# Performance work log

Measured on AMD Instinct MI355X. Metric: run time of the kernel, lower is better.

The kernel has to match this reference:

```python
import jax, jax.numpy as jnp
import numpy as np

NUM_HEADS = 12
EPS = 1e-4


def setup_inputs() -> dict:
    key = jax.random.key(0)
    k1, k2, k3 = jax.random.split(key, 3)
    C = 768
    B, N = 128, 196  # B = b * num_frames = 8 * 16
    x = jax.random.normal(k1, (B, N, C), dtype=jnp.float32)
    W_qkv = jax.random.normal(k2, (3 * C, C), dtype=jnp.float32) * 0.02
    W_proj = jax.random.normal(k3, (C, C), dtype=jnp.float32) * 0.02
    b_proj = jnp.zeros((C,), dtype=jnp.float32)
    return {"x": x, "W_qkv": W_qkv, "W_proj": W_proj, "b_proj": b_proj,
            "num_frames": 16}


def reference(x, W_qkv, W_proj, b_proj, num_frames):
    B, N, C = x.shape
    h = NUM_HEADS
    e = C // h
    # qkv projection (no bias), split k-first then heads: 'b n (k h e)'
    qkv = (x @ W_qkv.T).reshape(B, N, 3, h, e)
    q, k, v = qkv[:, :, 0], qkv[:, :, 1], qkv[:, :, 2]  # [B, N, h, e]
    q_ = jax.nn.relu(q)
    k_ = jax.nn.relu(k)
    # fold frames into the sequence: (b f) n -> b (f n)
    b = B // num_frames
    S = num_frames * N
    q_ = q_.reshape(b, S, h, e)
    k_ = k_.reshape(b, S, h, e)
    v_ = v.reshape(b, S, h, e)
    # kv trick: kv[b,h,e,d] = sum_s k[b,s,h,e] v[b,s,h,d]
    kv = jnp.einsum('bshe,bshd->bhed', k_, v_)
    k_sum = k_.sum(axis=1)  # [b, h, e]
    z = 1.0 / (jnp.einsum('bshe,bhe->bsh', q_, k_sum) + EPS)  # [b, S, h]
    out = jnp.einsum('bshe,bhed->bshd', q_, kv) * z[..., None]  # [b, S, h, e]
    out = out.reshape(B, N, C)
    # output projection (dropouts are identity at eval)
    return out @ W_proj.T + b_proj
```

## Files before the change

kernel.cpp:

```cpp
#include <hip/hip_runtime.h>
#include <hip/hip_bf16.h>

#define EPS_Z 1e-4f

typedef __attribute__((ext_vector_type(8))) short bf16x8;
typedef __attribute__((ext_vector_type(4))) float f32x4;

__device__ __forceinline__ float b2f(short s) {
    union { unsigned u; float f; } cv;
    cv.u = ((unsigned)(unsigned short)s) << 16;
    return cv.f;
}

__device__ __forceinline__ void gld_lds16(const __hip_bfloat16* g, __hip_bfloat16* l) {
    __builtin_amdgcn_global_load_lds(
        (__attribute__((address_space(1))) void*)(g),
        (__attribute__((address_space(3))) void*)(l),
        16, 0, 0);
}

__global__ __launch_bounds__(256)
void cvt_all(const float* __restrict__ x, const float* __restrict__ wq,
             const float* __restrict__ wp,
             __hip_bfloat16* __restrict__ xb, __hip_bfloat16* __restrict__ wqb,
             __hip_bfloat16* __restrict__ wpb)
{
    const int N4X = 25088 * 768 / 4;
    const int N4Q = 2304 * 768 / 4;
    const int N4P = 768 * 768 / 4;
    int i = blockIdx.x * 256 + threadIdx.x;
    const float* src;
    __hip_bfloat16* dst;
    int idx;
    if (i < N4X)            { src = x;  dst = xb;  idx = i; }
    else if (i < N4X + N4Q) { src = wq; dst = wqb; idx = i - N4X; }
    else if (i < N4X + N4Q + N4P) { src = wp; dst = wpb; idx = i - N4X - N4Q; }
    else return;
    float4 v = ((const float4*)src)[idx];
    union { short4 s; __hip_bfloat16 h[4]; } o;
    o.h[0] = __float2bfloat16(v.x);
    o.h[1] = __float2bfloat16(v.y);
    o.h[2] = __float2bfloat16(v.z);
    o.h[3] = __float2bfloat16(v.w);
    ((short4*)dst)[idx] = o.s;
}

template<int MODE, typename CT>
__global__ __launch_bounds__(256, 4)
void gemm_bt(const __hip_bfloat16* __restrict__ A,
             const __hip_bfloat16* __restrict__ B,
             CT* __restrict__ C,
             const float* __restrict__ bias,
             int K, int N, int gx)
{
    __shared__ __align__(16) __hip_bfloat16 As[128 * 64];
    __shared__ __align__(16) __hip_bfloat16 Bs[128 * 64];
    const int nwg = (int)gridDim.x;
    const int g = blockIdx.x;
    const int xcd = g & 7, lin = g >> 3;
    const int q = nwg >> 3, r = nwg & 7;
    const int gp = (xcd < r ? xcd * (q + 1) : r * (q + 1) + (xcd - r) * q) + lin;
    const int bx = gp % gx;
    const int by = gp / gx;

    const int tid = threadIdx.x;
    const int w = tid >> 6;
    const int l = tid & 63;
    const int wr = (w >> 1) * 64;
    const int wc = (w & 1) * 64;
    const int l15 = l & 15;
    const int lq = l >> 4;
    const int rx = l15 & 7;

    f32x4 acc[4][4] = {};

    const int srow8 = l >> 3;
    const int scol = (((l & 7) ^ (l >> 3)) << 3);

    const __hip_bfloat16* Ab = A + (size_t)by * 128 * K;
    const __hip_bfloat16* Bb = B + (size_t)bx * 128 * K;

    for (int k0 = 0; k0 < K; k0 += 64) {
        __syncthreads();
        #pragma unroll
        for (int i = 0; i < 4; ++i) {
            const int chunk = w * 4 + i;
            const int row = chunk * 8 + srow8;
            gld_lds16(Ab + (size_t)row * K + (k0 + scol), As + chunk * 512);
            gld_lds16(Bb + (size_t)row * K + (k0 + scol), Bs + chunk * 512);
        }
        __syncthreads();
        #pragma unroll
        for (int kk = 0; kk < 64; kk += 32) {
            const int kb = (kk >> 3) + lq;
            const int col = (kb ^ rx) << 3;
            bf16x8 a[4], b[4];
            #pragma unroll
            for (int i = 0; i < 4; ++i)
                a[i] = *(const bf16x8*)(As + (wr + i * 16 + l15) * 64 + col);
            #pragma unroll
            for (int j = 0; j < 4; ++j)
                b[j] = *(const bf16x8*)(Bs + (wc + j * 16 + l15) * 64 + col);
            #pragma unroll
            for (int i = 0; i < 4; ++i)
                #pragma unroll
                for (int j = 0; j < 4; ++j)
                    acc[i][j] = __builtin_amdgcn_mfma_f32_16x16x32_bf16(a[i], b[j], acc[i][j], 0, 0, 0);
        }
    }

    const int crow0 = by * 128 + wr + lq * 4;
    const int ccol0 = bx * 128 + wc + l15;
    #pragma unroll
    for (int i = 0; i < 4; ++i) {
        #pragma unroll
        for (int j = 0; j < 4; ++j) {
            const int gc = ccol0 + j * 16;
            const float badd = (MODE == 2) ? bias[gc] : 0.0f;
            #pragma unroll
            for (int r2 = 0; r2 < 4; ++r2) {
                const int gr = crow0 + i * 16 + r2;
                float v = acc[i][j][r2];
                if (MODE == 1 && gc < 1536) v = fmaxf(v, 0.0f);
                if (MODE == 2) v += badd;
                if (MODE == 1)
                    ((__hip_bfloat16*)C)[(size_t)gr * N + gc] = __float2bfloat16(v);
                else
                    ((float*)C)[(size_t)gr * N + gc] = v;
            }
        }
    }
}

__global__ __launch_bounds__(256)
void kv_mfma_kernel(const __hip_bfloat16* __restrict__ qkv,
                    float* __restrict__ kvp, float* __restrict__ ksump)
{
    const int SPLIT = 7;
    const int bh = blockIdx.x / SPLIT;
    const int ck = blockIdx.x % SPLIT;
    const int b = bh / 12, h = bh % 12;

    __shared__ __align__(16) __hip_bfloat16 kT[64 * 40];
    __shared__ __align__(16) __hip_bfloat16 vT[64 * 40];

    const int tid = threadIdx.x;
    const int w = tid >> 6, l = tid & 63;
    const int l15 = l & 15, lq = l >> 4;

    const int half = tid >> 7;
    const int idx  = tid & 127;
    const int e0 = (idx >> 4) * 8;
    const int sp = idx & 15;

    const size_t rowbase = (size_t)b * 3136 * 2304 + (half ? 1536 : 768) + h * 64 + e0;
    __hip_bfloat16* Tdst = half ? vT : kT;

    f32x4 acc[4] = {};
    f32x4 accks = {};

    bf16x8 ones;
    #pragma unroll
    for (int i = 0; i < 8; ++i) ones[i] = (short)0x3F80;

    const int s_begin = ck * 448;
    const int s_end = s_begin + 448;

    bf16x8 r0 = *(const bf16x8*)(qkv + rowbase + (size_t)(s_begin + 2 * sp) * 2304);
    bf16x8 r1 = *(const bf16x8*)(qkv + rowbase + (size_t)(s_begin + 2 * sp + 1) * 2304);

    for (int s0 = s_begin; s0 < s_end; s0 += 32) {
        __syncthreads();
        #pragma unroll
        for (int qq = 0; qq < 8; ++qq) {
            unsigned pk = ((unsigned)(unsigned short)r0[qq]) |
                          (((unsigned)(unsigned short)r1[qq]) << 16);
            *(unsigned*)(Tdst + (e0 + qq) * 40 + 2 * sp) = pk;
        }
        __syncthreads();
        if (s0 + 32 < s_end) {
            r0 = *(const bf16x8*)(qkv + rowbase + (size_t)(s0 + 32 + 2 * sp) * 2304);
            r1 = *(const bf16x8*)(qkv + rowbase + (size_t)(s0 + 33 + 2 * sp) * 2304);
        }
        bf16x8 a = *(const bf16x8*)(vT + (w * 16 + l15) * 40 + lq * 8);
        bf16x8 bfr[4];
        #pragma unroll
        for (int j = 0; j < 4; ++j)
            bfr[j] = *(const bf16x8*)(kT + (j * 16 + l15) * 40 + lq * 8);
        #pragma unroll
        for (int j = 0; j < 4; ++j)
            acc[j] = __builtin_amdgcn_mfma_f32_16x16x32_bf16(a, bfr[j], acc[j], 0, 0, 0);
        accks = __builtin_amdgcn_mfma_f32_16x16x32_bf16(ones, bfr[w], accks, 0, 0, 0);
    }

    float* kvdst = kvp + ((size_t)(bh * SPLIT + ck) << 12);
    #pragma unroll
    for (int j = 0; j < 4; ++j) {
        const int col = j * 16 + l15;
        #pragma unroll
        for (int r = 0; r < 4; ++r) {
            const int row = w * 16 + lq * 4 + r;
            kvdst[row * 64 + col] = acc[j][r];
        }
    }
    if (lq == 0)
        ksump[(size_t)(bh * SPLIT + ck) * 64 + w * 16 + l15] = accks[0];
}

__global__ __launch_bounds__(256)
void kv_reduce(const float* __restrict__ kvp, const float* __restrict__ ksump,
               __hip_bfloat16* __restrict__ kvb, float* __restrict__ ksum)
{
    const int SPLIT = 7;
    const int bh = blockIdx.x;
    const int tid = threadIdx.x;

    const float* base = kvp + ((size_t)bh * SPLIT << 12) + tid * 16;
    float4 s0 = {}, s1 = {}, s2 = {}, s3 = {};
    #pragma unroll
    for (int p = 0; p < SPLIT; ++p) {
        const float* bp = base + ((size_t)p << 12);
        float4 a0 = *(const float4*)(bp + 0);
        float4 a1 = *(const float4*)(bp + 4);
        float4 a2 = *(const float4*)(bp + 8);
        float4 a3 = *(const float4*)(bp + 12);
        s0.x += a0.x; s0.y += a0.y; s0.z += a0.z; s0.w += a0.w;
        s1.x += a1.x; s1.y += a1.y; s1.z += a1.z; s1.w += a1.w;
        s2.x += a2.x; s2.y += a2.y; s2.z += a2.z; s2.w += a2.w;
        s3.x += a3.x; s3.y += a3.y; s3.z += a3.z; s3.w += a3.w;
    }
    union { bf16x8 v; __hip_bfloat16 h[8]; } o0, o1;
    o0.h[0] = __float2bfloat16(s0.x); o0.h[1] = __float2bfloat16(s0.y);
    o0.h[2] = __float2bfloat16(s0.z); o0.h[3] = __float2bfloat16(s0.w);
    o0.h[4] = __float2bfloat16(s1.x); o0.h[5] = __float2bfloat16(s1.y);
    o0.h[6] = __float2bfloat16(s1.z); o0.h[7] = __float2bfloat16(s1.w);
    o1.h[0] = __float2bfloat16(s2.x); o1.h[1] = __float2bfloat16(s2.y);
    o1.h[2] = __float2bfloat16(s2.z); o1.h[3] = __float2bfloat16(s2.w);
    o1.h[4] = __float2bfloat16(s3.x); o1.h[5] = __float2bfloat16(s3.y);
    o1.h[6] = __float2bfloat16(s3.z); o1.h[7] = __float2bfloat16(s3.w);
    __hip_bfloat16* dst = kvb + ((size_t)bh << 12) + tid * 16;
    *(bf16x8*)(dst + 0) = o0.v;
    *(bf16x8*)(dst + 8) = o1.v;

    if (tid < 64) {
        float t = 0.0f;
        #pragma unroll
        for (int p = 0; p < SPLIT; ++p)
            t += ksump[(size_t)(bh * SPLIT + p) * 64 + tid];
        ksum[(size_t)bh * 64 + tid] = t;
    }
}

__global__ __launch_bounds__(128)
void attn_mfma3(const __hip_bfloat16* __restrict__ qkv,
                const __hip_bfloat16* __restrict__ kvb,
                const float* __restrict__ ksumg,
                __hip_bfloat16* __restrict__ att)
{
    const int x = blockIdx.x;
    const int b = x / 98;
    const int rem = x % 98;
    const int mt = rem >> 1, half = rem & 1;
    const int tid = threadIdx.x;
    const int w = tid >> 6, l = tid & 63;
    const int l15 = l & 15, lq = l >> 4;

    const size_t m0 = (size_t)b * 3136 + (size_t)mt * 64 + half * 32 + w * 16;

    #pragma unroll 1
    for (int h = 0; h < 12; ++h) {
        const int bh = b * 12 + h;

        const __hip_bfloat16* kvh = kvb + ((size_t)bh << 12);
        bf16x8 b0[4], b1[4];
        #pragma unroll
        for (int j = 0; j < 4; ++j) {
            b0[j] = *(const bf16x8*)(kvh + (j * 16 + l15) * 64 + lq * 8);
            b1[j] = *(const bf16x8*)(kvh + (j * 16 + l15) * 64 + 32 + lq * 8);
        }
        const float* ks = ksumg + (bh << 6);
        float kse[8], kse1[8];
        *(float4*)(kse)      = *(const float4*)(ks + lq * 8);
        *(float4*)(kse + 4)  = *(const float4*)(ks + lq * 8 + 4);
        *(float4*)(kse1)     = *(const float4*)(ks + 32 + lq * 8);
        *(float4*)(kse1 + 4) = *(const float4*)(ks + 32 + lq * 8 + 4);

        const __hip_bfloat16* qrow = qkv + (m0 + l15) * 2304 + h * 64;
        bf16x8 aq0 = *(const bf16x8*)(qrow + lq * 8);
        bf16x8 aq1 = *(const bf16x8*)(qrow + 32 + lq * 8);

        float zp = 0.0f;
        #pragma unroll
        for (int j = 0; j < 8; ++j)
            zp += b2f(aq0[j]) * kse[j] + b2f(aq1[j]) * kse1[j];
        zp += __shfl_xor(zp, 16);
        zp += __shfl_xor(zp, 32);
        const float zr = 1.0f / (zp + EPS_Z);

        f32x4 acc[4] = {};
        #pragma unroll
        for (int j = 0; j < 4; ++j) {
            acc[j] = __builtin_amdgcn_mfma_f32_16x16x32_bf16(aq0, b0[j], acc[j], 0, 0, 0);
            acc[j] = __builtin_amdgcn_mfma_f32_16x16x32_bf16(aq1, b1[j], acc[j], 0, 0, 0);
        }

        float zrow[4];
        #pragma unroll
        for (int r = 0; r < 4; ++r) zrow[r] = __shfl(zr, lq * 4 + r);

        #pragma unroll
        for (int j = 0; j < 4; ++j) {
            const int col = j * 16 + l15;
            #pragma unroll
            for (int r = 0; r < 4; ++r) {
                const int row = lq * 4 + r;
                att[(m0 + row) * 768 + h * 64 + col] = __float2bfloat16(acc[j][r] * zrow[r]);
            }
        }
    }
}

extern "C" void kernel_launch(void* const* d_in, const int* in_sizes, int n_in,
                              void* d_out, int out_size, void* d_ws, size_t ws_size,
                              hipStream_t stream)
{
    const float* x      = (const float*)d_in[0];
    const float* W_qkv  = (const float*)d_in[1];
    const float* W_proj = (const float*)d_in[2];
    const float* b_proj = (const float*)d_in[3];
    float* out = (float*)d_out;

    const int M = 25088, K = 768, N1 = 2304, N2 = 768;
    const int SPLIT = 7;
    const int MH = M / 2;

    __hip_bfloat16* qkv = (__hip_bfloat16*)d_ws;
    __hip_bfloat16* xb  = qkv + (size_t)M * N1;
    __hip_bfloat16* wqb = xb + (size_t)M * K;
    __hip_bfloat16* wpb = wqb + (size_t)N1 * K;
    float* kvp   = (float*)(wpb + (size_t)N2 * K);
    float* ksump = kvp + (size_t)SPLIT * 96 * 4096;
    float* ksum  = ksump + (size_t)SPLIT * 96 * 64;
    __hip_bfloat16* kvb = (__hip_bfloat16*)(ksum + 96 * 64);
    __hip_bfloat16* att = xb;

    const int CVT_TOT = (M * K + N1 * K + N2 * K) / 4;
    cvt_all<<<(CVT_TOT + 255) / 256, 256, 0, stream>>>(x, W_qkv, W_proj, xb, wqb, wpb);

    gemm_bt<1, __hip_bfloat16><<<(MH / 128) * (N1 / 128), 256, 0, stream>>>(
        xb, wqb, qkv, nullptr, K, N1, N1 / 128);
    gemm_bt<1, __hip_bfloat16><<<(MH / 128) * (N1 / 128), 256, 0, stream>>>(
        xb + (size_t)MH * K, wqb, qkv + (size_t)MH * N1, nullptr, K, N1, N1 / 128);

    kv_mfma_kernel<<<96 * SPLIT, 256, 0, stream>>>(qkv, kvp, ksump);
    kv_reduce<<<96, 256, 0, stream>>>(kvp, ksump, kvb, ksum);
    attn_mfma3<<<784, 128, 0, stream>>>(qkv, kvb, ksum, att);
    gemm_bt<2, float><<<(M / 128) * (N2 / 128), 256, 0, stream>>>(
        att, wpb, out, b_proj, K, N2, N2 / 128);
}
```

Measured before the change: 360.4 us.

## Fuse attention output with projection GEMM and merge split QKV GEMM launches

```diff
diff --git a/kernel.cpp b/kernel.cpp
--- a/kernel.cpp
+++ b/kernel.cpp
@@ -46,7 +46,7 @@
 }
 
 template<int MODE, typename CT>
-__global__ __launch_bounds__(256, 4)
+__global__ __launch_bounds__(256, 3)
 void gemm_bt(const __hip_bfloat16* __restrict__ A,
              const __hip_bfloat16* __restrict__ B,
              CT* __restrict__ C,
@@ -251,32 +251,35 @@
     }
 }
 
-__global__ __launch_bounds__(128)
-void attn_mfma3(const __hip_bfloat16* __restrict__ qkv,
-                const __hip_bfloat16* __restrict__ kvb,
-                const float* __restrict__ ksumg,
-                __hip_bfloat16* __restrict__ att)
-{
-    const int x = blockIdx.x;
-    const int b = x / 98;
-    const int rem = x % 98;
-    const int mt = rem >> 1, half = rem & 1;
+__global__ __launch_bounds__(256, 3)
+void attn_proj(const __hip_bfloat16* __restrict__ qkv,
+               const __hip_bfloat16* __restrict__ kvb,
+               const float* __restrict__ ksumg,
+               const __hip_bfloat16* __restrict__ wpb,
+               const float* __restrict__ bias,
+               float* __restrict__ out)
+{
+    __shared__ __align__(16) __hip_bfloat16 att_s[32 * 776];
+
+    const int blk = blockIdx.x;
+    const size_t m0 = (size_t)blk * 32;
+    const int bidx = (int)(m0 / 3136);
     const int tid = threadIdx.x;
     const int w = tid >> 6, l = tid & 63;
     const int l15 = l & 15, lq = l >> 4;
-
-    const size_t m0 = (size_t)b * 3136 + (size_t)mt * 64 + half * 32 + w * 16;
+    const int rt = w & 1;
+    const int ch = w >> 1;
 
     #pragma unroll 1
     for (int h = 0; h < 12; ++h) {
-        const int bh = b * 12 + h;
-
+        const int bh = bidx * 12 + h;
         const __hip_bfloat16* kvh = kvb + ((size_t)bh << 12);
-        bf16x8 b0[4], b1[4];
-        #pragma unroll
-        for (int j = 0; j < 4; ++j) {
-            b0[j] = *(const bf16x8*)(kvh + (j * 16 + l15) * 64 + lq * 8);
-            b1[j] = *(const bf16x8*)(kvh + (j * 16 + l15) * 64 + 32 + lq * 8);
+        bf16x8 b0[2], b1[2];
+        #pragma unroll
+        for (int j = 0; j < 2; ++j) {
+            const int col = ch * 32 + j * 16 + l15;
+            b0[j] = *(const bf16x8*)(kvh + col * 64 + lq * 8);
+            b1[j] = *(const bf16x8*)(kvh + col * 64 + 32 + lq * 8);
         }
         const float* ks = ksumg + (bh << 6);
         float kse[8], kse1[8];
@@ -285,7 +288,7 @@
         *(float4*)(kse1)     = *(const float4*)(ks + 32 + lq * 8);
         *(float4*)(kse1 + 4) = *(const float4*)(ks + 32 + lq * 8 + 4);
 
-        const __hip_bfloat16* qrow = qkv + (m0 + l15) * 2304 + h * 64;
+        const __hip_bfloat16* qrow = qkv + (m0 + rt * 16 + l15) * 2304 + h * 64;
         bf16x8 aq0 = *(const bf16x8*)(qrow + lq * 8);
         bf16x8 aq1 = *(const bf16x8*)(qrow + 32 + lq * 8);
 
@@ -297,11 +300,11 @@
         zp += __shfl_xor(zp, 32);
         const float zr = 1.0f / (zp + EPS_Z);
 
-        f32x4 acc[4] = {};
-        #pragma unroll
-        for (int j = 0; j < 4; ++j) {
-            acc[j] = __builtin_amdgcn_mfma_f32_16x16x32_bf16(aq0, b0[j], acc[j], 0, 0, 0);
-            acc[j] = __builtin_amdgcn_mfma_f32_16x16x32_bf16(aq1, b1[j], acc[j], 0, 0, 0);
+        f32x4 pacc[2] = {};
+        #pragma unroll
+        for (int j = 0; j < 2; ++j) {
+            pacc[j] = __builtin_amdgcn_mfma_f32_16x16x32_bf16(aq0, b0[j], pacc[j], 0, 0, 0);
+            pacc[j] = __builtin_amdgcn_mfma_f32_16x16x32_bf16(aq1, b1[j], pacc[j], 0, 0, 0);
         }
 
         float zrow[4];
@@ -309,12 +312,46 @@
         for (int r = 0; r < 4; ++r) zrow[r] = __shfl(zr, lq * 4 + r);
 
         #pragma unroll
-        for (int j = 0; j < 4; ++j) {
-            const int col = j * 16 + l15;
+        for (int j = 0; j < 2; ++j) {
+            const int col = h * 64 + ch * 32 + j * 16 + l15;
             #pragma unroll
             for (int r = 0; r < 4; ++r) {
-                const int row = lq * 4 + r;
-                att[(m0 + row) * 768 + h * 64 + col] = __float2bfloat16(acc[j][r] * zrow[r]);
+                const int row = rt * 16 + lq * 4 + r;
+                att_s[row * 776 + col] = __float2bfloat16(pacc[j][r] * zrow[r]);
+            }
+        }
+    }
+    __syncthreads();
+
+    #pragma unroll 1
+    for (int pass = 0; pass < 2; ++pass) {
+        const int c0 = w * 192 + pass * 96;
+        f32x4 acc[2][6] = {};
+        #pragma unroll 1
+        for (int k0 = 0; k0 < 768; k0 += 32) {
+            bf16x8 a0 = *(const bf16x8*)(att_s + (0 * 16 + l15) * 776 + k0 + lq * 8);
+            bf16x8 a1 = *(const bf16x8*)(att_s + (1 * 16 + l15) * 776 + k0 + lq * 8);
+            bf16x8 bf[6];
+            #pragma unroll
+            for (int j = 0; j < 6; ++j)
+                bf[j] = *(const bf16x8*)(wpb + (size_t)(c0 + j * 16 + l15) * 768 + k0 + lq * 8);
+            #pragma unroll
+            for (int j = 0; j < 6; ++j) {
+                acc[0][j] = __builtin_amdgcn_mfma_f32_16x16x32_bf16(a0, bf[j], acc[0][j], 0, 0, 0);
+                acc[1][j] = __builtin_amdgcn_mfma_f32_16x16x32_bf16(a1, bf[j], acc[1][j], 0, 0, 0);
+            }
+        }
+        #pragma unroll
+        for (int j = 0; j < 6; ++j) {
+            const int gc = c0 + j * 16 + l15;
+            const float badd = bias[gc];
+            #pragma unroll
+            for (int rt2 = 0; rt2 < 2; ++rt2) {
+                #pragma unroll
+                for (int r = 0; r < 4; ++r) {
+                    const size_t gr = m0 + rt2 * 16 + lq * 4 + r;
+                    out[gr * 768 + gc] = acc[rt2][j][r] + badd;
+                }
             }
         }
     }
@@ -332,7 +369,6 @@
 
     const int M = 25088, K = 768, N1 = 2304, N2 = 768;
     const int SPLIT = 7;
-    const int MH = M / 2;
 
     __hip_bfloat16* qkv = (__hip_bfloat16*)d_ws;
     __hip_bfloat16* xb  = qkv + (size_t)M * N1;
@@ -342,19 +378,14 @@
     float* ksump = kvp + (size_t)SPLIT * 96 * 4096;
     float* ksum  = ksump + (size_t)SPLIT * 96 * 64;
     __hip_bfloat16* kvb = (__hip_bfloat16*)(ksum + 96 * 64);
-    __hip_bfloat16* att = xb;
 
     const int CVT_TOT = (M * K + N1 * K + N2 * K) / 4;
     cvt_all<<<(CVT_TOT + 255) / 256, 256, 0, stream>>>(x, W_qkv, W_proj, xb, wqb, wpb);
 
-    gemm_bt<1, __hip_bfloat16><<<(MH / 128) * (N1 / 128), 256, 0, stream>>>(
+    gemm_bt<1, __hip_bfloat16><<<(M / 128) * (N1 / 128), 256, 0, stream>>>(
         xb, wqb, qkv, nullptr, K, N1, N1 / 128);
-    gemm_bt<1, __hip_bfloat16><<<(MH / 128) * (N1 / 128), 256, 0, stream>>>(
-        xb + (size_t)MH * K, wqb, qkv + (size_t)MH * N1, nullptr, K, N1, N1 / 128);
 
     kv_mfma_kernel<<<96 * SPLIT, 256, 0, stream>>>(qkv, kvp, ksump);
     kv_reduce<<<96, 256, 0, stream>>>(kvp, ksump, kvb, ksum);
-    attn_mfma3<<<784, 128, 0, stream>>>(qkv, kvb, ksum, att);
-    gemm_bt<2, float><<<(M / 128) * (N2 / 128), 256, 0, stream>>>(
-        att, wpb, out, b_proj, K, N2, N2 / 128);
-}
+    attn_proj<<<M / 32, 256, 0, stream>>>(qkv, kvb, ksum, wpb, b_proj, out);
+}
```

Result: slower. 458.5 us (+27.2%).
